# Optimization experiments

Measured on AMD Instinct MI355X. Metric: run time of the kernel, lower is better.

Reference implementation:

```python
import jax, jax.numpy as jnp
import numpy as np

EMBED_DIM = 1024
NUM_HEADS = 16
HEAD_DIM = EMBED_DIM // NUM_HEADS
B, S = 4, 2048


def setup_inputs() -> dict:
    key = jax.random.key(0)
    ks = jax.random.split(key, 9)
    scale = 1.0 / np.sqrt(EMBED_DIM)
    x = jax.random.normal(ks[0], (B, S, EMBED_DIM), dtype=jnp.float32)
    Wq = jax.random.normal(ks[1], (EMBED_DIM, EMBED_DIM), dtype=jnp.float32) * scale
    Wk = jax.random.normal(ks[2], (EMBED_DIM, EMBED_DIM), dtype=jnp.float32) * scale
    Wv = jax.random.normal(ks[3], (EMBED_DIM, EMBED_DIM), dtype=jnp.float32) * scale
    Wo = jax.random.normal(ks[4], (EMBED_DIM, EMBED_DIM), dtype=jnp.float32) * scale
    bq = jnp.zeros((EMBED_DIM,), jnp.float32)
    bk = jnp.zeros((EMBED_DIM,), jnp.float32)
    bv = jnp.zeros((EMBED_DIM,), jnp.float32)
    bo = jnp.zeros((EMBED_DIM,), jnp.float32)
    return {"x": x, "Wq": Wq, "bq": bq, "Wk": Wk, "bk": bk, "Wv": Wv, "bv": bv, "Wo": Wo, "bo": bo}


def _split_heads(t):
    # [B,S,E] -> [B,H,S,D]
    b, s, _ = t.shape
    return t.reshape(b, s, NUM_HEADS, HEAD_DIM).transpose(0, 2, 1, 3)


def reference(x, Wq, bq, Wk, bk, Wv, bv, Wo, bo):
    q = _split_heads(x @ Wq + bq)
    k = _split_heads(x @ Wk + bk)
    v = _split_heads(x @ Wv + bv)
    scale = 1.0 / jnp.sqrt(jnp.asarray(HEAD_DIM, x.dtype))
    scores = jnp.einsum('bhqd,bhkd->bhqk', q, k) * scale  # [B,H,S,S]
    weights = jax.nn.softmax(scores, axis=-1)
    attn = jnp.einsum('bhqk,bhkd->bhqd', weights, v)  # [B,H,S,D]
    b, h, s, d = attn.shape
    concat = attn.transpose(0, 2, 1, 3).reshape(b, s, h * d)
    return concat @ Wo + bo
```

## Files before the change

### kernel.cpp

```cpp
#include <hip/hip_runtime.h>
#include <hip/hip_bf16.h>

typedef unsigned short u16;
typedef __attribute__((ext_vector_type(8))) short bf16x8;
typedef __attribute__((ext_vector_type(4))) float f32x4;
typedef __attribute__((ext_vector_type(4))) unsigned short u16x4;

#define EMB 1024
#define SEQ 2048
#define NH 16
#define HD 64

#define OFF_WT   0u
#define OFF_WOT  3145728u
#define OFF_Q    4194304u
#define OFF_K    12582912u
#define OFF_VT   20971520u
#define OFF_OC   29360128u

#define QSCALE 0.1803368801111f

__device__ __forceinline__ u16 f2bf(float f) {
    unsigned int x; __builtin_memcpy(&x, &f, 4);
    unsigned int r = x + 0x7fffu + ((x >> 16) & 1u);
    return (u16)(r >> 16);
}

#if defined(__has_builtin) && __has_builtin(__builtin_amdgcn_cvt_pk_bf16_f32)
typedef __attribute__((ext_vector_type(2))) __bf16 bfv2;
__device__ __forceinline__ unsigned int pkbf(float a, float b) {
    bfv2 v = __builtin_amdgcn_cvt_pk_bf16_f32(a, b);
    unsigned int u; __builtin_memcpy(&u, &v, 4); return u;
}
#else
__device__ __forceinline__ unsigned int pkbf(float a, float b) {
    return (unsigned)f2bf(a) | ((unsigned)f2bf(b) << 16);
}
#endif

#if defined(__has_builtin) && __has_builtin(__builtin_amdgcn_exp2f)
__device__ __forceinline__ float exp2fast(float x) { return __builtin_amdgcn_exp2f(x); }
#else
__device__ __forceinline__ float exp2fast(float x) { return __builtin_exp2f(x); }
#endif

__device__ __forceinline__ void gld_lds16(const void* gsrc, void* ldst) {
    void* g = const_cast<void*>(gsrc);
    __builtin_amdgcn_global_load_lds((__attribute__((address_space(1))) void*)g,
                                     (__attribute__((address_space(3))) void*)ldst,
                                     16, 0, 0);
}

__global__ __launch_bounds__(256) void convert_x(
    const float* __restrict__ x, u16* __restrict__ xb)
{
    int i = (blockIdx.x * 256 + threadIdx.x) * 4;
    float4 v = *(const float4*)&x[i];
    uint2 o = { pkbf(v.x, v.y), pkbf(v.z, v.w) };
    *(uint2*)&xb[i] = o;
}

__global__ __launch_bounds__(256) void transpose_w(
    const float* __restrict__ W0, const float* __restrict__ W1,
    const float* __restrict__ W2, const float* __restrict__ W3,
    u16* __restrict__ ws)
{
    __shared__ u16 tile[64 * 65];
    const float* src = blockIdx.z == 0 ? W0 : blockIdx.z == 1 ? W1 : blockIdx.z == 2 ? W2 : W3;
    u16* dst = ws + (blockIdx.z < 3 ? (unsigned)blockIdx.z * 1048576u : OFF_WOT);
    const int k0 = blockIdx.x * 64, n0 = blockIdx.y * 64;
    const int t = threadIdx.x;
    #pragma unroll
    for (int i = 0; i < 16; i++) {
        int idx = i * 256 + t; int r = idx >> 6, c = idx & 63;
        tile[c * 65 + r] = f2bf(src[(k0 + r) * EMB + n0 + c]);
    }
    __syncthreads();
    #pragma unroll
    for (int i = 0; i < 16; i++) {
        int idx = i * 256 + t; int r = idx >> 6, c = idx & 63;
        dst[(n0 + r) * EMB + k0 + c] = tile[r * 65 + c];
    }
}

__global__ __launch_bounds__(256) void gemm_qkv(
    const u16* __restrict__ X, const u16* __restrict__ WT,
    const float* __restrict__ bq, const float* __restrict__ bk, const float* __restrict__ bv,
    u16* __restrict__ Qt, u16* __restrict__ Ko, u16* __restrict__ Vt)
{
    __shared__ u16 Al[128 * 32];
    __shared__ u16 Bl[128 * 32];
    const int t = threadIdx.x, lane = t & 63, w = t >> 6;
    const int quad = lane >> 4, l15 = lane & 15;
    const int wr = w >> 1, wc = w & 1;
    const int m0 = blockIdx.x * 128, n0 = blockIdx.y * 128;
    const f32x4 fzero = {0.f, 0.f, 0.f, 0.f};

    f32x4 acc[4][4];
    #pragma unroll
    for (int i = 0; i < 4; i++)
        #pragma unroll
        for (int j = 0; j < 4; j++) acc[i][j] = fzero;

    for (int kt = 0; kt < 32; ++kt) {
        #pragma unroll
        for (int r = 0; r < 2; r++) {
            int g = r * 256 + t; int row = g >> 2, cw = g & 3;
            int sc = (cw ^ ((row >> 1) & 3)) * 8;
            gld_lds16(X  + (size_t)(m0 + row) * EMB + kt * 32 + sc, &Al[g * 8]);
            gld_lds16(WT + (size_t)(n0 + row) * EMB + kt * 32 + sc, &Bl[g * 8]);
        }
        __syncthreads();
        bf16x8 af[4], bfr[4];
        #pragma unroll
        for (int i = 0; i < 4; i++) {
            int rowA = wr * 64 + i * 16 + l15;
            af[i] = *(const bf16x8*)&Al[rowA * 32 + ((quad ^ ((rowA >> 1) & 3)) * 8)];
        }
        #pragma unroll
        for (int j = 0; j < 4; j++) {
            int rowB = wc * 64 + j * 16 + l15;
            bfr[j] = *(const bf16x8*)&Bl[rowB * 32 + ((quad ^ ((rowB >> 1) & 3)) * 8)];
        }
        #pragma unroll
        for (int i = 0; i < 4; i++)
            #pragma unroll
            for (int j = 0; j < 4; j++)
                acc[i][j] = __builtin_amdgcn_mfma_f32_16x16x32_bf16(af[i], bfr[j], acc[i][j], 0, 0, 0);
        __syncthreads();
    }

    const int seg = n0 >> 10;
    const float* bias = seg == 0 ? bq : (seg == 1 ? bk : bv);
    #pragma unroll
    for (int j = 0; j < 4; j++) {
        int n = n0 + wc * 64 + j * 16 + l15;
        int nn = n & 1023;
        float bvl = bias[nn];
        int h = nn >> 6, d = nn & 63;
        #pragma unroll
        for (int i = 0; i < 4; i++) {
            int m = m0 + wr * 64 + i * 16 + quad * 4;
            int b = m >> 11, s = m & 2047;
            if (seg == 0) {
                uint2 pp = { pkbf((acc[i][j][0] + bvl) * QSCALE, (acc[i][j][1] + bvl) * QSCALE),
                             pkbf((acc[i][j][2] + bvl) * QSCALE, (acc[i][j][3] + bvl) * QSCALE) };
                *(uint2*)&Qt[(size_t)((b * NH + h) * HD + d) * SEQ + s] = pp;
            } else if (seg == 2) {
                uint2 pp = { pkbf(acc[i][j][0] + bvl, acc[i][j][1] + bvl),
                             pkbf(acc[i][j][2] + bvl, acc[i][j][3] + bvl) };
                *(uint2*)&Vt[(size_t)((b * NH + h) * HD + d) * SEQ + s] = pp;
            } else {
                size_t base = (size_t)((b * NH + h) * SEQ + s) * HD + d;
                #pragma unroll
                for (int r = 0; r < 4; r++) Ko[base + (size_t)r * HD] = f2bf(acc[i][j][r] + bvl);
            }
        }
    }
}

__global__ __launch_bounds__(256, 2) void flash_attn(
    const u16* __restrict__ Q, const u16* __restrict__ K,
    const u16* __restrict__ VT, u16* __restrict__ Oc)
{
    __shared__ u16 Kl[64 * 64];
    __shared__ u16 Vl[64 * 64];
    __shared__ u16 Pl[4 * 64 * 72];
    const int t = threadIdx.x, lane = t & 63, w = t >> 6;
    const int quad = lane >> 4, l15 = lane & 15;
    const int a7 = l15 & 7;
    const int bh = blockIdx.y;
    const int b = bh >> 4, h = bh & 15;
    const int q0 = blockIdx.x * 256 + w * 64;
    const u16* Qtb = Q + (size_t)bh * HD * SEQ;
    const u16* Kb  = K + (size_t)bh * SEQ * HD;
    const u16* Vb  = VT + (size_t)bh * HD * SEQ;
    const f32x4 fzero = {0.f, 0.f, 0.f, 0.f};

    const u16* kbase0 = &Kl[l15 * 64 + ((quad ^ a7) * 8)];
    const u16* kbase1 = &Kl[l15 * 64 + (((4 + quad) ^ a7) * 8)];
    const u16* vbase0 = &Vl[l15 * 64 + ((quad ^ a7) * 8)];
    const u16* vbase1 = &Vl[l15 * 64 + (((4 + quad) ^ a7) * 8)];
    u16* Pw = &Pl[w * 64 * 72];
    u16* pww = Pw + l15 * 72 + quad * 4;
    const u16* pwr = Pw + l15 * 72 + quad * 8;

    bf16x8 ones;
    #pragma unroll
    for (int j = 0; j < 8; j++) ones[j] = (short)0x3F80;

    bf16x8 qf[4][2];
    #pragma unroll
    for (int i = 0; i < 4; i++)
        #pragma unroll
        for (int c = 0; c < 2; c++)
            #pragma unroll
            for (int j = 0; j < 8; j++)
                qf[i][c][j] = (short)Qtb[(size_t)(c * 32 + quad * 8 + j) * SEQ + q0 + i * 16 + l15];

    f32x4 oacc[4][4];
    f32x4 oextra[4];
    #pragma unroll
    for (int i = 0; i < 4; i++) {
        oextra[i] = fzero;
        #pragma unroll
        for (int f = 0; f < 4; f++) oacc[i][f] = fzero;
    }

    for (int kt = 0; kt < 32; ++kt) {
        #pragma unroll
        for (int r = 0; r < 2; r++) {
            int g = r * 256 + t, row = g >> 3, cw = g & 7;
            int swz = (cw ^ (row & 7)) * 8;
            gld_lds16(Kb + (size_t)kt * 64 * HD + row * HD + swz, &Kl[g * 8]);
            gld_lds16(Vb + (size_t)row * SEQ + kt * 64 + swz, &Vl[g * 8]);
        }
        __syncthreads();

        {
            bf16x8 ak[2][4];
            #pragma unroll
            for (int f = 0; f < 4; f++) {
                ak[0][f] = *(const bf16x8*)(kbase0 + f * 1024);
                ak[1][f] = *(const bf16x8*)(kbase1 + f * 1024);
            }
            #pragma unroll
            for (int i = 0; i < 4; i++) {
                f32x4 sf[4];
                #pragma unroll
                for (int f = 0; f < 4; f++) sf[f] = fzero;
                #pragma unroll
                for (int c = 0; c < 2; c++)
                    #pragma unroll
                    for (int f = 0; f < 4; f++)
                        sf[f] = __builtin_amdgcn_mfma_f32_16x16x32_bf16(ak[c][f], qf[i][c], sf[f], 0, 0, 0);
                #pragma unroll
                for (int f = 0; f < 4; f++) {
                    float p0 = exp2fast(sf[f][0]);
                    float p1 = exp2fast(sf[f][1]);
                    float p2 = exp2fast(sf[f][2]);
                    float p3 = exp2fast(sf[f][3]);
                    uint2 pp = { pkbf(p0, p1), pkbf(p2, p3) };
                    *(uint2*)(pww + i * 1152 + f * 16) = pp;
                }
            }
        }

        {
            bf16x8 av[2][4];
            #pragma unroll
            for (int f = 0; f < 4; f++) {
                av[0][f] = *(const bf16x8*)(vbase0 + f * 1024);
                av[1][f] = *(const bf16x8*)(vbase1 + f * 1024);
            }
            #pragma unroll
            for (int i = 0; i < 4; i++) {
                bf16x8 bp0 = *(const bf16x8*)(pwr + i * 1152);
                bf16x8 bp1 = *(const bf16x8*)(pwr + i * 1152 + 32);
                #pragma unroll
                for (int f = 0; f < 4; f++) {
                    oacc[i][f] = __builtin_amdgcn_mfma_f32_16x16x32_bf16(av[0][f], bp0, oacc[i][f], 0, 0, 0);
                    oacc[i][f] = __builtin_amdgcn_mfma_f32_16x16x32_bf16(av[1][f], bp1, oacc[i][f], 0, 0, 0);
                }
                oextra[i] = __builtin_amdgcn_mfma_f32_16x16x32_bf16(ones, bp0, oextra[i], 0, 0, 0);
                oextra[i] = __builtin_amdgcn_mfma_f32_16x16x32_bf16(ones, bp1, oextra[i], 0, 0, 0);
            }
        }
        __syncthreads();
    }

    #pragma unroll
    for (int i = 0; i < 4; i++) {
        float inv = 1.0f / oextra[i][0];
        int s = q0 + i * 16 + l15;
        size_t base = ((size_t)(b * SEQ + s) * NH + h) * HD;
        #pragma unroll
        for (int f = 0; f < 4; f++) {
            uint2 o = { pkbf(oacc[i][f][0] * inv, oacc[i][f][1] * inv),
                        pkbf(oacc[i][f][2] * inv, oacc[i][f][3] * inv) };
            *(uint2*)&Oc[base + f * 16 + quad * 4] = o;
        }
    }
}

__global__ __launch_bounds__(256) void gemm_out(
    const u16* __restrict__ A, const u16* __restrict__ WT,
    const float* __restrict__ bo, float* __restrict__ out)
{
    __shared__ u16 Al[128 * 32];
    __shared__ u16 Bl[128 * 32];
    const int t = threadIdx.x, lane = t & 63, w = t >> 6;
    const int quad = lane >> 4, l15 = lane & 15;
    const int wr = w >> 1, wc = w & 1;
    const int m0 = blockIdx.x * 128, n0 = blockIdx.y * 128;
    const f32x4 fzero = {0.f, 0.f, 0.f, 0.f};

    f32x4 acc[4][4];
    #pragma unroll
    for (int i = 0; i < 4; i++)
        #pragma unroll
        for (int j = 0; j < 4; j++) acc[i][j] = fzero;

    for (int kt = 0; kt < 32; ++kt) {
        #pragma unroll
        for (int r = 0; r < 2; r++) {
            int g = r * 256 + t; int row = g >> 2, cw = g & 3;
            int sc = (cw ^ ((row >> 1) & 3)) * 8;
            gld_lds16(A  + (size_t)(m0 + row) * EMB + kt * 32 + sc, &Al[g * 8]);
            gld_lds16(WT + (size_t)(n0 + row) * EMB + kt * 32 + sc, &Bl[g * 8]);
        }
        __syncthreads();
        bf16x8 af[4], bfr[4];
        #pragma unroll
        for (int i = 0; i < 4; i++) {
            int rowA = wr * 64 + i * 16 + l15;
            af[i] = *(const bf16x8*)&Al[rowA * 32 + ((quad ^ ((rowA >> 1) & 3)) * 8)];
        }
        #pragma unroll
        for (int j = 0; j < 4; j++) {
            int rowB = wc * 64 + j * 16 + l15;
            bfr[j] = *(const bf16x8*)&Bl[rowB * 32 + ((quad ^ ((rowB >> 1) & 3)) * 8)];
        }
        #pragma unroll
        for (int i = 0; i < 4; i++)
            #pragma unroll
            for (int j = 0; j < 4; j++)
                acc[i][j] = __builtin_amdgcn_mfma_f32_16x16x32_bf16(af[i], bfr[j], acc[i][j], 0, 0, 0);
        __syncthreads();
    }

    #pragma unroll
    for (int j = 0; j < 4; j++) {
        int n = n0 + wc * 64 + j * 16 + l15;
        float bvl = bo[n];
        #pragma unroll
        for (int i = 0; i < 4; i++) {
            int m = m0 + wr * 64 + i * 16 + quad * 4;
            #pragma unroll
            for (int r = 0; r < 4; r++)
                out[(size_t)(m + r) * EMB + n] = acc[i][j][r] + bvl;
        }
    }
}

extern "C" void kernel_launch(void* const* d_in, const int* in_sizes, int n_in,
                              void* d_out, int out_size, void* d_ws, size_t ws_size,
                              hipStream_t stream)
{
    (void)in_sizes; (void)n_in; (void)out_size; (void)ws_size;
    const float* x  = (const float*)d_in[0];
    const float* Wq = (const float*)d_in[1];
    const float* bq = (const float*)d_in[2];
    const float* Wk = (const float*)d_in[3];
    const float* bk = (const float*)d_in[4];
    const float* Wv = (const float*)d_in[5];
    const float* bv = (const float*)d_in[6];
    const float* Wo = (const float*)d_in[7];
    const float* bo = (const float*)d_in[8];
    u16* ws = (u16*)d_ws;
    u16* Xb = (u16*)d_out;

    convert_x<<<dim3(8192), 256, 0, stream>>>(x, Xb);
    transpose_w<<<dim3(16, 16, 4), 256, 0, stream>>>(Wq, Wk, Wv, Wo, ws);
    gemm_qkv<<<dim3(64, 24), 256, 0, stream>>>(Xb, ws + OFF_WT, bq, bk, bv,
                                               ws + OFF_Q, ws + OFF_K, ws + OFF_VT);
    flash_attn<<<dim3(8, 64), 256, 0, stream>>>(ws + OFF_Q, ws + OFF_K,
                                                ws + OFF_VT, ws + OFF_OC);
    gemm_out<<<dim3(64, 8), 256, 0, stream>>>(ws + OFF_OC, ws + OFF_WOT, bo, (float*)d_out);
}
```

Before: 291.1 us.

## Prefetch next tile into LDS while computing on register fragments

In all three kernels, the LDS fragments for the current tile are read into registers, then the block syncs and issues the global-to-LDS loads for the next tile before running the MFMA compute. The aim is to overlap global memory latency with matrix math instead of stalling on each load before compute. Address computation is hoisted out of the loop into precomputed per-thread source pointers. Each iteration now has two barriers and full waitcnt drains, and register pressure rises in flash_attn because K and V fragments stay live together.

```diff
diff --git a/kernel.cpp b/kernel.cpp
--- a/kernel.cpp
+++ b/kernel.cpp
@@ -19,6 +19,8 @@
 #define OFF_OC   29360128u
 
 #define QSCALE 0.1803368801111f
+
+#define FULL_DRAIN() __builtin_amdgcn_s_waitcnt(0)
 
 __device__ __forceinline__ u16 f2bf(float f) {
     unsigned int x; __builtin_memcpy(&x, &f, 4);
@@ -96,20 +98,27 @@
     const int m0 = blockIdx.x * 128, n0 = blockIdx.y * 128;
     const f32x4 fzero = {0.f, 0.f, 0.f, 0.f};
 
+    const int gA = t, gB = 256 + t;
+    const int rA = gA >> 2, scA = ((gA & 3) ^ ((rA >> 1) & 3)) * 8;
+    const int rB = gB >> 2, scB = ((gB & 3) ^ ((rB >> 1) & 3)) * 8;
+    const u16* xs0 = X  + (size_t)(m0 + rA) * EMB + scA;
+    const u16* xs1 = X  + (size_t)(m0 + rB) * EMB + scB;
+    const u16* ws0 = WT + (size_t)(n0 + rA) * EMB + scA;
+    const u16* ws1 = WT + (size_t)(n0 + rB) * EMB + scB;
+
     f32x4 acc[4][4];
     #pragma unroll
     for (int i = 0; i < 4; i++)
         #pragma unroll
         for (int j = 0; j < 4; j++) acc[i][j] = fzero;
 
+    gld_lds16(xs0, &Al[gA * 8]);
+    gld_lds16(xs1, &Al[gB * 8]);
+    gld_lds16(ws0, &Bl[gA * 8]);
+    gld_lds16(ws1, &Bl[gB * 8]);
+
     for (int kt = 0; kt < 32; ++kt) {
-        #pragma unroll
-        for (int r = 0; r < 2; r++) {
-            int g = r * 256 + t; int row = g >> 2, cw = g & 3;
-            int sc = (cw ^ ((row >> 1) & 3)) * 8;
-            gld_lds16(X  + (size_t)(m0 + row) * EMB + kt * 32 + sc, &Al[g * 8]);
-            gld_lds16(WT + (size_t)(n0 + row) * EMB + kt * 32 + sc, &Bl[g * 8]);
-        }
+        FULL_DRAIN();
         __syncthreads();
         bf16x8 af[4], bfr[4];
         #pragma unroll
@@ -122,12 +131,20 @@
             int rowB = wc * 64 + j * 16 + l15;
             bfr[j] = *(const bf16x8*)&Bl[rowB * 32 + ((quad ^ ((rowB >> 1) & 3)) * 8)];
         }
+        FULL_DRAIN();
+        __syncthreads();
+        if (kt + 1 < 32) {
+            const int o = (kt + 1) * 32;
+            gld_lds16(xs0 + o, &Al[gA * 8]);
+            gld_lds16(xs1 + o, &Al[gB * 8]);
+            gld_lds16(ws0 + o, &Bl[gA * 8]);
+            gld_lds16(ws1 + o, &Bl[gB * 8]);
+        }
         #pragma unroll
         for (int i = 0; i < 4; i++)
             #pragma unroll
             for (int j = 0; j < 4; j++)
                 acc[i][j] = __builtin_amdgcn_mfma_f32_16x16x32_bf16(af[i], bfr[j], acc[i][j], 0, 0, 0);
-        __syncthreads();
     }
 
     const int seg = n0 >> 10;
@@ -177,6 +194,14 @@
     const u16* Vb  = VT + (size_t)bh * HD * SEQ;
     const f32x4 fzero = {0.f, 0.f, 0.f, 0.f};
 
+    const int g0 = t, g1 = 256 + t;
+    const int r0 = g0 >> 3, sz0 = ((g0 & 7) ^ (r0 & 7)) * 8;
+    const int r1 = g1 >> 3, sz1 = ((g1 & 7) ^ (r1 & 7)) * 8;
+    const u16* ksrc0 = Kb + r0 * HD + sz0;
+    const u16* ksrc1 = Kb + r1 * HD + sz1;
+    const u16* vsrc0 = Vb + (size_t)r0 * SEQ + sz0;
+    const u16* vsrc1 = Vb + (size_t)r1 * SEQ + sz1;
+
     const u16* kbase0 = &Kl[l15 * 64 + ((quad ^ a7) * 8)];
     const u16* kbase1 = &Kl[l15 * 64 + (((4 + quad) ^ a7) * 8)];
     const u16* vbase0 = &Vl[l15 * 64 + ((quad ^ a7) * 8)];
@@ -207,66 +232,69 @@
         for (int f = 0; f < 4; f++) oacc[i][f] = fzero;
     }
 
+    gld_lds16(ksrc0, &Kl[g0 * 8]);
+    gld_lds16(ksrc1, &Kl[g1 * 8]);
+    gld_lds16(vsrc0, &Vl[g0 * 8]);
+    gld_lds16(vsrc1, &Vl[g1 * 8]);
+
     for (int kt = 0; kt < 32; ++kt) {
-        #pragma unroll
-        for (int r = 0; r < 2; r++) {
-            int g = r * 256 + t, row = g >> 3, cw = g & 7;
-            int swz = (cw ^ (row & 7)) * 8;
-            gld_lds16(Kb + (size_t)kt * 64 * HD + row * HD + swz, &Kl[g * 8]);
-            gld_lds16(Vb + (size_t)row * SEQ + kt * 64 + swz, &Vl[g * 8]);
-        }
-        __syncthreads();
-
-        {
-            bf16x8 ak[2][4];
+        FULL_DRAIN();
+        __syncthreads();
+
+        bf16x8 ak[2][4], av[2][4];
+        #pragma unroll
+        for (int f = 0; f < 4; f++) {
+            ak[0][f] = *(const bf16x8*)(kbase0 + f * 1024);
+            ak[1][f] = *(const bf16x8*)(kbase1 + f * 1024);
+            av[0][f] = *(const bf16x8*)(vbase0 + f * 1024);
+            av[1][f] = *(const bf16x8*)(vbase1 + f * 1024);
+        }
+
+        FULL_DRAIN();
+        __syncthreads();
+
+        if (kt + 1 < 32) {
+            const int ko = (kt + 1) * 4096;
+            const int vo = (kt + 1) * 64;
+            gld_lds16(ksrc0 + ko, &Kl[g0 * 8]);
+            gld_lds16(ksrc1 + ko, &Kl[g1 * 8]);
+            gld_lds16(vsrc0 + vo, &Vl[g0 * 8]);
+            gld_lds16(vsrc1 + vo, &Vl[g1 * 8]);
+        }
+
+        #pragma unroll
+        for (int i = 0; i < 4; i++) {
+            f32x4 sf[4];
+            #pragma unroll
+            for (int f = 0; f < 4; f++) sf[f] = fzero;
+            #pragma unroll
+            for (int c = 0; c < 2; c++)
+                #pragma unroll
+                for (int f = 0; f < 4; f++)
+                    sf[f] = __builtin_amdgcn_mfma_f32_16x16x32_bf16(ak[c][f], qf[i][c], sf[f], 0, 0, 0);
             #pragma unroll
             for (int f = 0; f < 4; f++) {
-                ak[0][f] = *(const bf16x8*)(kbase0 + f * 1024);
-                ak[1][f] = *(const bf16x8*)(kbase1 + f * 1024);
+                float p0 = exp2fast(sf[f][0]);
+                float p1 = exp2fast(sf[f][1]);
+                float p2 = exp2fast(sf[f][2]);
+                float p3 = exp2fast(sf[f][3]);
+                uint2 pp = { pkbf(p0, p1), pkbf(p2, p3) };
+                *(uint2*)(pww + i * 1152 + f * 16) = pp;
             }
-            #pragma unroll
-            for (int i = 0; i < 4; i++) {
-                f32x4 sf[4];
-                #pragma unroll
-                for (int f = 0; f < 4; f++) sf[f] = fzero;
-                #pragma unroll
-                for (int c = 0; c < 2; c++)
-                    #pragma unroll
-                    for (int f = 0; f < 4; f++)
-                        sf[f] = __builtin_amdgcn_mfma_f32_16x16x32_bf16(ak[c][f], qf[i][c], sf[f], 0, 0, 0);
-                #pragma unroll
-                for (int f = 0; f < 4; f++) {
-                    float p0 = exp2fast(sf[f][0]);
-                    float p1 = exp2fast(sf[f][1]);
-                    float p2 = exp2fast(sf[f][2]);
-                    float p3 = exp2fast(sf[f][3]);
-                    uint2 pp = { pkbf(p0, p1), pkbf(p2, p3) };
-                    *(uint2*)(pww + i * 1152 + f * 16) = pp;
-                }
+        }
+
+        #pragma unroll
+        for (int i = 0; i < 4; i++) {
+            bf16x8 bp0 = *(const bf16x8*)(pwr + i * 1152);
+            bf16x8 bp1 = *(const bf16x8*)(pwr + i * 1152 + 32);
+            #pragma unroll
+            for (int f = 0; f < 4; f++) {
+                oacc[i][f] = __builtin_amdgcn_mfma_f32_16x16x32_bf16(av[0][f], bp0, oacc[i][f], 0, 0, 0);
+                oacc[i][f] = __builtin_amdgcn_mfma_f32_16x16x32_bf16(av[1][f], bp1, oacc[i][f], 0, 0, 0);
             }
-        }
-
-        {
-            bf16x8 av[2][4];
-            #pragma unroll
-            for (int f = 0; f < 4; f++) {
-                av[0][f] = *(const bf16x8*)(vbase0 + f * 1024);
-                av[1][f] = *(const bf16x8*)(vbase1 + f * 1024);
-            }
-            #pragma unroll
-            for (int i = 0; i < 4; i++) {
-                bf16x8 bp0 = *(const bf16x8*)(pwr + i * 1152);
-                bf16x8 bp1 = *(const bf16x8*)(pwr + i * 1152 + 32);
-                #pragma unroll
-                for (int f = 0; f < 4; f++) {
-                    oacc[i][f] = __builtin_amdgcn_mfma_f32_16x16x32_bf16(av[0][f], bp0, oacc[i][f], 0, 0, 0);
-                    oacc[i][f] = __builtin_amdgcn_mfma_f32_16x16x32_bf16(av[1][f], bp1, oacc[i][f], 0, 0, 0);
-                }
-                oextra[i] = __builtin_amdgcn_mfma_f32_16x16x32_bf16(ones, bp0, oextra[i], 0, 0, 0);
-                oextra[i] = __builtin_amdgcn_mfma_f32_16x16x32_bf16(ones, bp1, oextra[i], 0, 0, 0);
-            }
-        }
-        __syncthreads();
+            oextra[i] = __builtin_amdgcn_mfma_f32_16x16x32_bf16(ones, bp0, oextra[i], 0, 0, 0);
+            oextra[i] = __builtin_amdgcn_mfma_f32_16x16x32_bf16(ones, bp1, oextra[i], 0, 0, 0);
+        }
     }
 
     #pragma unroll
@@ -295,20 +323,27 @@
     const int m0 = blockIdx.x * 128, n0 = blockIdx.y * 128;
     const f32x4 fzero = {0.f, 0.f, 0.f, 0.f};
 
+    const int gA = t, gB = 256 + t;
+    const int rA = gA >> 2, scA = ((gA & 3) ^ ((rA >> 1) & 3)) * 8;
+    const int rB = gB >> 2, scB = ((gB & 3) ^ ((rB >> 1) & 3)) * 8;
+    const u16* as0 = A  + (size_t)(m0 + rA) * EMB + scA;
+    const u16* as1 = A  + (size_t)(m0 + rB) * EMB + scB;
+    const u16* bs0 = WT + (size_t)(n0 + rA) * EMB + scA;
+    const u16* bs1 = WT + (size_t)(n0 + rB) * EMB + scB;
+
     f32x4 acc[4][4];
     #pragma unroll
     for (int i = 0; i < 4; i++)
         #pragma unroll
         for (int j = 0; j < 4; j++) acc[i][j] = fzero;
 
+    gld_lds16(as0, &Al[gA * 8]);
+    gld_lds16(as1, &Al[gB * 8]);
+    gld_lds16(bs0, &Bl[gA * 8]);
+    gld_lds16(bs1, &Bl[gB * 8]);
+
     for (int kt = 0; kt < 32; ++kt) {
-        #pragma unroll
-        for (int r = 0; r < 2; r++) {
-            int g = r * 256 + t; int row = g >> 2, cw = g & 3;
-            int sc = (cw ^ ((row >> 1) & 3)) * 8;
-            gld_lds16(A  + (size_t)(m0 + row) * EMB + kt * 32 + sc, &Al[g * 8]);
-            gld_lds16(WT + (size_t)(n0 + row) * EMB + kt * 32 + sc, &Bl[g * 8]);
-        }
+        FULL_DRAIN();
         __syncthreads();
         bf16x8 af[4], bfr[4];
         #pragma unroll
@@ -321,12 +356,20 @@
             int rowB = wc * 64 + j * 16 + l15;
             bfr[j] = *(const bf16x8*)&Bl[rowB * 32 + ((quad ^ ((rowB >> 1) & 3)) * 8)];
         }
+        FULL_DRAIN();
+        __syncthreads();
+        if (kt + 1 < 32) {
+            const int o = (kt + 1) * 32;
+            gld_lds16(as0 + o, &Al[gA * 8]);
+            gld_lds16(as1 + o, &Al[gB * 8]);
+            gld_lds16(bs0 + o, &Bl[gA * 8]);
+            gld_lds16(bs1 + o, &Bl[gB * 8]);
+        }
         #pragma unroll
         for (int i = 0; i < 4; i++)
             #pragma unroll
             for (int j = 0; j < 4; j++)
                 acc[i][j] = __builtin_amdgcn_mfma_f32_16x16x32_bf16(af[i], bfr[j], acc[i][j], 0, 0, 0);
-        __syncthreads();
     }
 
     #pragma unroll
```

Measured after the change: 291.5 us. About the same (+0.2%).

## Widen GEMM K-tiles to 64 and prefetch next K/V tile in flash attention

Applied to the files above, without the earlier changes.

The QKV and output GEMMs now stage 64-wide K slices with an 8-way XOR swizzle, which halves the number of loop iterations and barriers per tile. The flash attention loop loads K and V fragments into registers at the top of each iteration, then issues the global-to-LDS loads for the next tile before running the QK, exp and PV math. The aim is to overlap memory latency with MFMA work in a single LDS buffer. In exchange the GEMMs use twice the LDS, the attention kernel holds more registers for the live V fragments, and an added full waitcnt drain and extra barrier run every iteration.

```diff
diff --git a/kernel.cpp b/kernel.cpp
--- a/kernel.cpp
+++ b/kernel.cpp
@@ -20,6 +20,8 @@
 
 #define QSCALE 0.1803368801111f
 
+#define FULL_DRAIN() __builtin_amdgcn_s_waitcnt(0)
+
 __device__ __forceinline__ u16 f2bf(float f) {
     unsigned int x; __builtin_memcpy(&x, &f, 4);
     unsigned int r = x + 0x7fffu + ((x >> 16) & 1u);
@@ -88,45 +90,59 @@
     const float* __restrict__ bq, const float* __restrict__ bk, const float* __restrict__ bv,
     u16* __restrict__ Qt, u16* __restrict__ Ko, u16* __restrict__ Vt)
 {
-    __shared__ u16 Al[128 * 32];
-    __shared__ u16 Bl[128 * 32];
+    __shared__ u16 Al[128 * 64];
+    __shared__ u16 Bl[128 * 64];
     const int t = threadIdx.x, lane = t & 63, w = t >> 6;
     const int quad = lane >> 4, l15 = lane & 15;
+    const int a7 = l15 & 7;
     const int wr = w >> 1, wc = w & 1;
     const int m0 = blockIdx.x * 128, n0 = blockIdx.y * 128;
     const f32x4 fzero = {0.f, 0.f, 0.f, 0.f};
 
+    const u16* abase0 = &Al[(wr * 64 + l15) * 64 + ((quad ^ a7) * 8)];
+    const u16* abase1 = &Al[(wr * 64 + l15) * 64 + (((4 + quad) ^ a7) * 8)];
+    const u16* bbase0 = &Bl[(wc * 64 + l15) * 64 + ((quad ^ a7) * 8)];
+    const u16* bbase1 = &Bl[(wc * 64 + l15) * 64 + (((4 + quad) ^ a7) * 8)];
+
     f32x4 acc[4][4];
     #pragma unroll
     for (int i = 0; i < 4; i++)
         #pragma unroll
         for (int j = 0; j < 4; j++) acc[i][j] = fzero;
 
-    for (int kt = 0; kt < 32; ++kt) {
-        #pragma unroll
-        for (int r = 0; r < 2; r++) {
-            int g = r * 256 + t; int row = g >> 2, cw = g & 3;
-            int sc = (cw ^ ((row >> 1) & 3)) * 8;
-            gld_lds16(X  + (size_t)(m0 + row) * EMB + kt * 32 + sc, &Al[g * 8]);
-            gld_lds16(WT + (size_t)(n0 + row) * EMB + kt * 32 + sc, &Bl[g * 8]);
-        }
-        __syncthreads();
-        bf16x8 af[4], bfr[4];
-        #pragma unroll
-        for (int i = 0; i < 4; i++) {
-            int rowA = wr * 64 + i * 16 + l15;
-            af[i] = *(const bf16x8*)&Al[rowA * 32 + ((quad ^ ((rowA >> 1) & 3)) * 8)];
-        }
-        #pragma unroll
-        for (int j = 0; j < 4; j++) {
-            int rowB = wc * 64 + j * 16 + l15;
-            bfr[j] = *(const bf16x8*)&Bl[rowB * 32 + ((quad ^ ((rowB >> 1) & 3)) * 8)];
-        }
-        #pragma unroll
-        for (int i = 0; i < 4; i++)
-            #pragma unroll
-            for (int j = 0; j < 4; j++)
-                acc[i][j] = __builtin_amdgcn_mfma_f32_16x16x32_bf16(af[i], bfr[j], acc[i][j], 0, 0, 0);
+    for (int kt = 0; kt < 16; ++kt) {
+        #pragma unroll
+        for (int r = 0; r < 4; r++) {
+            int g = r * 256 + t; int row = g >> 3, cw = g & 7;
+            int sc = (cw ^ (row & 7)) * 8;
+            gld_lds16(X  + (size_t)(m0 + row) * EMB + kt * 64 + sc, &Al[g * 8]);
+            gld_lds16(WT + (size_t)(n0 + row) * EMB + kt * 64 + sc, &Bl[g * 8]);
+        }
+        __syncthreads();
+        {
+            bf16x8 af[4], bfr[4];
+            #pragma unroll
+            for (int i = 0; i < 4; i++) af[i] = *(const bf16x8*)(abase0 + i * 1024);
+            #pragma unroll
+            for (int j = 0; j < 4; j++) bfr[j] = *(const bf16x8*)(bbase0 + j * 1024);
+            #pragma unroll
+            for (int i = 0; i < 4; i++)
+                #pragma unroll
+                for (int j = 0; j < 4; j++)
+                    acc[i][j] = __builtin_amdgcn_mfma_f32_16x16x32_bf16(af[i], bfr[j], acc[i][j], 0, 0, 0);
+        }
+        {
+            bf16x8 af[4], bfr[4];
+            #pragma unroll
+            for (int i = 0; i < 4; i++) af[i] = *(const bf16x8*)(abase1 + i * 1024);
+            #pragma unroll
+            for (int j = 0; j < 4; j++) bfr[j] = *(const bf16x8*)(bbase1 + j * 1024);
+            #pragma unroll
+            for (int i = 0; i < 4; i++)
+                #pragma unroll
+                for (int j = 0; j < 4; j++)
+                    acc[i][j] = __builtin_amdgcn_mfma_f32_16x16x32_bf16(af[i], bfr[j], acc[i][j], 0, 0, 0);
+        }
         __syncthreads();
     }
 
@@ -177,6 +193,14 @@
     const u16* Vb  = VT + (size_t)bh * HD * SEQ;
     const f32x4 fzero = {0.f, 0.f, 0.f, 0.f};
 
+    const int g0 = t, g1 = 256 + t;
+    const int r0 = g0 >> 3, sz0 = ((g0 & 7) ^ (r0 & 7)) * 8;
+    const int r1 = g1 >> 3, sz1 = ((g1 & 7) ^ (r1 & 7)) * 8;
+    const u16* ksrc0 = Kb + r0 * HD + sz0;
+    const u16* ksrc1 = Kb + r1 * HD + sz1;
+    const u16* vsrc0 = Vb + (size_t)r0 * SEQ + sz0;
+    const u16* vsrc1 = Vb + (size_t)r1 * SEQ + sz1;
+
     const u16* kbase0 = &Kl[l15 * 64 + ((quad ^ a7) * 8)];
     const u16* kbase1 = &Kl[l15 * 64 + (((4 + quad) ^ a7) * 8)];
     const u16* vbase0 = &Vl[l15 * 64 + ((quad ^ a7) * 8)];
@@ -207,66 +231,69 @@
         for (int f = 0; f < 4; f++) oacc[i][f] = fzero;
     }
 
+    gld_lds16(ksrc0, &Kl[g0 * 8]);
+    gld_lds16(ksrc1, &Kl[g1 * 8]);
+    gld_lds16(vsrc0, &Vl[g0 * 8]);
+    gld_lds16(vsrc1, &Vl[g1 * 8]);
+
     for (int kt = 0; kt < 32; ++kt) {
-        #pragma unroll
-        for (int r = 0; r < 2; r++) {
-            int g = r * 256 + t, row = g >> 3, cw = g & 7;
-            int swz = (cw ^ (row & 7)) * 8;
-            gld_lds16(Kb + (size_t)kt * 64 * HD + row * HD + swz, &Kl[g * 8]);
-            gld_lds16(Vb + (size_t)row * SEQ + kt * 64 + swz, &Vl[g * 8]);
-        }
-        __syncthreads();
-
-        {
-            bf16x8 ak[2][4];
+        FULL_DRAIN();
+        __syncthreads();
+
+        bf16x8 ak[2][4], av[2][4];
+        #pragma unroll
+        for (int f = 0; f < 4; f++) {
+            ak[0][f] = *(const bf16x8*)(kbase0 + f * 1024);
+            ak[1][f] = *(const bf16x8*)(kbase1 + f * 1024);
+            av[0][f] = *(const bf16x8*)(vbase0 + f * 1024);
+            av[1][f] = *(const bf16x8*)(vbase1 + f * 1024);
+        }
+
+        FULL_DRAIN();
+        __syncthreads();
+
+        if (kt + 1 < 32) {
+            const int ko = (kt + 1) * 4096;
+            const int vo = (kt + 1) * 64;
+            gld_lds16(ksrc0 + ko, &Kl[g0 * 8]);
+            gld_lds16(ksrc1 + ko, &Kl[g1 * 8]);
+            gld_lds16(vsrc0 + vo, &Vl[g0 * 8]);
+            gld_lds16(vsrc1 + vo, &Vl[g1 * 8]);
+        }
+
+        #pragma unroll
+        for (int i = 0; i < 4; i++) {
+            f32x4 sf[4];
+            #pragma unroll
+            for (int f = 0; f < 4; f++) sf[f] = fzero;
+            #pragma unroll
+            for (int c = 0; c < 2; c++)
+                #pragma unroll
+                for (int f = 0; f < 4; f++)
+                    sf[f] = __builtin_amdgcn_mfma_f32_16x16x32_bf16(ak[c][f], qf[i][c], sf[f], 0, 0, 0);
             #pragma unroll
             for (int f = 0; f < 4; f++) {
-                ak[0][f] = *(const bf16x8*)(kbase0 + f * 1024);
-                ak[1][f] = *(const bf16x8*)(kbase1 + f * 1024);
+                float p0 = exp2fast(sf[f][0]);
+                float p1 = exp2fast(sf[f][1]);
+                float p2 = exp2fast(sf[f][2]);
+                float p3 = exp2fast(sf[f][3]);
+                uint2 pp = { pkbf(p0, p1), pkbf(p2, p3) };
+                *(uint2*)(pww + i * 1152 + f * 16) = pp;
             }
-            #pragma unroll
-            for (int i = 0; i < 4; i++) {
-                f32x4 sf[4];
-                #pragma unroll
-                for (int f = 0; f < 4; f++) sf[f] = fzero;
-                #pragma unroll
-                for (int c = 0; c < 2; c++)
-                    #pragma unroll
-                    for (int f = 0; f < 4; f++)
-                        sf[f] = __builtin_amdgcn_mfma_f32_16x16x32_bf16(ak[c][f], qf[i][c], sf[f], 0, 0, 0);
-                #pragma unroll
-                for (int f = 0; f < 4; f++) {
-                    float p0 = exp2fast(sf[f][0]);
-                    float p1 = exp2fast(sf[f][1]);
-                    float p2 = exp2fast(sf[f][2]);
-                    float p3 = exp2fast(sf[f][3]);
-                    uint2 pp = { pkbf(p0, p1), pkbf(p2, p3) };
-                    *(uint2*)(pww + i * 1152 + f * 16) = pp;
-                }
+        }
+
+        #pragma unroll
+        for (int i = 0; i < 4; i++) {
+            bf16x8 bp0 = *(const bf16x8*)(pwr + i * 1152);
+            bf16x8 bp1 = *(const bf16x8*)(pwr + i * 1152 + 32);
+            #pragma unroll
+            for (int f = 0; f < 4; f++) {
+                oacc[i][f] = __builtin_amdgcn_mfma_f32_16x16x32_bf16(av[0][f], bp0, oacc[i][f], 0, 0, 0);
+                oacc[i][f] = __builtin_amdgcn_mfma_f32_16x16x32_bf16(av[1][f], bp1, oacc[i][f], 0, 0, 0);
             }
-        }
-
-        {
-            bf16x8 av[2][4];
-            #pragma unroll
-            for (int f = 0; f < 4; f++) {
-                av[0][f] = *(const bf16x8*)(vbase0 + f * 1024);
-                av[1][f] = *(const bf16x8*)(vbase1 + f * 1024);
-            }
-            #pragma unroll
-            for (int i = 0; i < 4; i++) {
-                bf16x8 bp0 = *(const bf16x8*)(pwr + i * 1152);
-                bf16x8 bp1 = *(const bf16x8*)(pwr + i * 1152 + 32);
-                #pragma unroll
-                for (int f = 0; f < 4; f++) {
-                    oacc[i][f] = __builtin_amdgcn_mfma_f32_16x16x32_bf16(av[0][f], bp0, oacc[i][f], 0, 0, 0);
-                    oacc[i][f] = __builtin_amdgcn_mfma_f32_16x16x32_bf16(av[1][f], bp1, oacc[i][f], 0, 0, 0);
-                }
-                oextra[i] = __builtin_amdgcn_mfma_f32_16x16x32_bf16(ones, bp0, oextra[i], 0, 0, 0);
-                oextra[i] = __builtin_amdgcn_mfma_f32_16x16x32_bf16(ones, bp1, oextra[i], 0, 0, 0);
-            }
-        }
-        __syncthreads();
+            oextra[i] = __builtin_amdgcn_mfma_f32_16x16x32_bf16(ones, bp0, oextra[i], 0, 0, 0);
+            oextra[i] = __builtin_amdgcn_mfma_f32_16x16x32_bf16(ones, bp1, oextra[i], 0, 0, 0);
+        }
     }
 
     #pragma unroll
@@ -287,45 +314,59 @@
     const u16* __restrict__ A, const u16* __restrict__ WT,
     const float* __restrict__ bo, float* __restrict__ out)
 {
-    __shared__ u16 Al[128 * 32];
-    __shared__ u16 Bl[128 * 32];
+    __shared__ u16 Al[128 * 64];
+    __shared__ u16 Bl[128 * 64];
     const int t = threadIdx.x, lane = t & 63, w = t >> 6;
     const int quad = lane >> 4, l15 = lane & 15;
+    const int a7 = l15 & 7;
     const int wr = w >> 1, wc = w & 1;
     const int m0 = blockIdx.x * 128, n0 = blockIdx.y * 128;
     const f32x4 fzero = {0.f, 0.f, 0.f, 0.f};
 
+    const u16* abase0 = &Al[(wr * 64 + l15) * 64 + ((quad ^ a7) * 8)];
+    const u16* abase1 = &Al[(wr * 64 + l15) * 64 + (((4 + quad) ^ a7) * 8)];
+    const u16* bbase0 = &Bl[(wc * 64 + l15) * 64 + ((quad ^ a7) * 8)];
+    const u16* bbase1 = &Bl[(wc * 64 + l15) * 64 + (((4 + quad) ^ a7) * 8)];
+
     f32x4 acc[4][4];
     #pragma unroll
     for (int i = 0; i < 4; i++)
         #pragma unroll
         for (int j = 0; j < 4; j++) acc[i][j] = fzero;
 
-    for (int kt = 0; kt < 32; ++kt) {
-        #pragma unroll
-        for (int r = 0; r < 2; r++) {
-            int g = r * 256 + t; int row = g >> 2, cw = g & 3;
-            int sc = (cw ^ ((row >> 1) & 3)) * 8;
-            gld_lds16(A  + (size_t)(m0 + row) * EMB + kt * 32 + sc, &Al[g * 8]);
-            gld_lds16(WT + (size_t)(n0 + row) * EMB + kt * 32 + sc, &Bl[g * 8]);
-        }
-        __syncthreads();
-        bf16x8 af[4], bfr[4];
-        #pragma unroll
-        for (int i = 0; i < 4; i++) {
-            int rowA = wr * 64 + i * 16 + l15;
-            af[i] = *(const bf16x8*)&Al[rowA * 32 + ((quad ^ ((rowA >> 1) & 3)) * 8)];
-        }
-        #pragma unroll
-        for (int j = 0; j < 4; j++) {
-            int rowB = wc * 64 + j * 16 + l15;
-            bfr[j] = *(const bf16x8*)&Bl[rowB * 32 + ((quad ^ ((rowB >> 1) & 3)) * 8)];
-        }
-        #pragma unroll
-        for (int i = 0; i < 4; i++)
-            #pragma unroll
-            for (int j = 0; j < 4; j++)
-                acc[i][j] = __builtin_amdgcn_mfma_f32_16x16x32_bf16(af[i], bfr[j], acc[i][j], 0, 0, 0);
+    for (int kt = 0; kt < 16; ++kt) {
+        #pragma unroll
+        for (int r = 0; r < 4; r++) {
+            int g = r * 256 + t; int row = g >> 3, cw = g & 7;
+            int sc = (cw ^ (row & 7)) * 8;
+            gld_lds16(A  + (size_t)(m0 + row) * EMB + kt * 64 + sc, &Al[g * 8]);
+            gld_lds16(WT + (size_t)(n0 + row) * EMB + kt * 64 + sc, &Bl[g * 8]);
+        }
+        __syncthreads();
+        {
+            bf16x8 af[4], bfr[4];
+            #pragma unroll
+            for (int i = 0; i < 4; i++) af[i] = *(const bf16x8*)(abase0 + i * 1024);
+            #pragma unroll
+            for (int j = 0; j < 4; j++) bfr[j] = *(const bf16x8*)(bbase0 + j * 1024);
+            #pragma unroll
+            for (int i = 0; i < 4; i++)
+                #pragma unroll
+                for (int j = 0; j < 4; j++)
+                    acc[i][j] = __builtin_amdgcn_mfma_f32_16x16x32_bf16(af[i], bfr[j], acc[i][j], 0, 0, 0);
+        }
+        {
+            bf16x8 af[4], bfr[4];
+            #pragma unroll
+            for (int i = 0; i < 4; i++) af[i] = *(const bf16x8*)(abase1 + i * 1024);
+            #pragma unroll
+            for (int j = 0; j < 4; j++) bfr[j] = *(const bf16x8*)(bbase1 + j * 1024);
+            #pragma unroll
+            for (int i = 0; i < 4; i++)
+                #pragma unroll
+                for (int j = 0; j < 4; j++)
+                    acc[i][j] = __builtin_amdgcn_mfma_f32_16x16x32_bf16(af[i], bfr[j], acc[i][j], 0, 0, 0);
+        }
         __syncthreads();
     }
 
```

Result: no change. 291.3 us (+0.1%).
